# Optimization experiments

Measured on AMD Instinct MI355X. Metric: run time of the kernel, lower is better.

The kernel has to match this reference:

```python
import jax, jax.numpy as jnp
import numpy as np

NUM_HEADS = 16
NUM_KV_HEADS = 4
HEAD_DIM = 128
BATCH = 4
SEQ = 2048  # equal per-sequence length; cu_seqlens = arange(BATCH+1)*SEQ


def setup_inputs() -> dict:
    key = jax.random.key(0)
    k1, k2, k3 = jax.random.split(key, 3)
    T = BATCH * SEQ
    q = jax.random.normal(k1, (T, NUM_HEADS * HEAD_DIM), dtype=jnp.float32)
    k = jax.random.normal(k2, (T, NUM_KV_HEADS * HEAD_DIM), dtype=jnp.float32)
    v = jax.random.normal(k3, (T, NUM_KV_HEADS * HEAD_DIM), dtype=jnp.float32)
    cu = jnp.arange(BATCH + 1, dtype=jnp.int32) * SEQ
    return {"q": q, "k": k, "v": v, "cu_seqlens_q": cu, "cu_seqlens_k": cu}


def reference(q, k, v, cu_seqlens_q, cu_seqlens_k):
    # Prefill varlen causal attention with GQA (block_tables=None path).
    # Sequences have equal length, so the ragged batch reshapes to dense [B,S,...].
    B = cu_seqlens_q.shape[0] - 1
    T = q.shape[0]
    S = T // B
    D = HEAD_DIM
    G = NUM_HEADS // NUM_KV_HEADS  # GQA group size
    qh = q.reshape(B, S, NUM_KV_HEADS, G, D)
    kh = k.reshape(B, S, NUM_KV_HEADS, D)
    vh = v.reshape(B, S, NUM_KV_HEADS, D)
    scale = 1.0 / np.sqrt(D).astype(np.float32)  # SDPA scale=None default
    # scores: [B, Hkv, G, Sq, Sk]
    scores = jnp.einsum('bqhgd,bkhd->bhgqk', qh, kh) * scale
    causal = jnp.tril(jnp.ones((S, S), dtype=bool))
    scores = jnp.where(causal, scores, jnp.finfo(scores.dtype).min)
    probs = jax.nn.softmax(scores, axis=-1)
    o = jnp.einsum('bhgqk,bkhd->bqhgd', probs, vh)
    return o.reshape(T, NUM_HEADS * HEAD_DIM)
```

## Files before the change

### kernel.cpp

```cpp
#include <hip/hip_runtime.h>


typedef __attribute__((ext_vector_type(8))) short bs8;
typedef __attribute__((ext_vector_type(16))) float f16x;
typedef __attribute__((ext_vector_type(4))) unsigned int u32x4;
typedef __attribute__((ext_vector_type(4))) unsigned short u16x4;
typedef unsigned short u16;
typedef unsigned int u32;

#define B_ 4
#define S_ 2048
#define HQ_ 16
#define HKV_ 4
#define NQT 16
#define NKT_TOT 32
#define TILE_ELEMS 8192

__device__ __forceinline__ u16 f2bf(float f) {
  u32 u = __float_as_uint(f);
  u += 0x7fffu + ((u >> 16) & 1u);
  return (u16)(u >> 16);
}

__global__ void pack_k(const float* __restrict__ k, u16* __restrict__ kp) {
  int g = blockIdx.x * 256 + threadIdx.x;
  int row = g >> 7;
  int col = (g & 127) << 2;
  int h = col >> 7, d0 = col & 127;
  int b = row >> 11, s = row & 2047;
  int kt = s >> 6, kv = s & 63;
  float4 vv = *(const float4*)(k + (size_t)row * 512 + col);
  int ti = (b * HKV_ + h) * NKT_TOT + kt;
  int e = kv * 128 + (d0 ^ (8 * (kv & 15)));
  u16x4 o;
  o.x = f2bf(vv.x); o.y = f2bf(vv.y); o.z = f2bf(vv.z); o.w = f2bf(vv.w);
  *(u16x4*)(kp + (size_t)ti * TILE_ELEMS + e) = o;
}

__global__ void pack_v(const float* __restrict__ v, u16* __restrict__ vp) {
  __shared__ u16 img[TILE_ELEMS];
  int ti = blockIdx.x;
  int kt = ti & 31;
  int bh = ti >> 5;
  int h = bh & 3, b = bh >> 2;
  int t = threadIdx.x;
#pragma unroll
  for (int p = 0; p < 8; ++p) {
    int t2 = p * 256 + t;
    int kvr = t2 >> 5;
    int d0 = (t2 & 31) << 2;
    float4 vv = *(const float4*)(v + (size_t)(b * S_ + kt * 64 + kvr) * 512 + h * 128 + d0);
    float a[4] = {vv.x, vv.y, vv.z, vv.w};
#pragma unroll
    for (int j = 0; j < 4; ++j) {
      int d = d0 + j;
      img[(d >> 1) * 128 + (d & 1) * 64 + (kvr ^ (8 * ((d >> 1) & 7)))] = f2bf(a[j]);
    }
  }
  __syncthreads();
#pragma unroll
  for (int p = 0; p < 4; ++p) {
    int e0 = (p * 256 + t) * 8;
    *(bs8*)(vp + (size_t)ti * TILE_ELEMS + e0) = *(const bs8*)&img[e0];
  }
}

__device__ __forceinline__ void gl2lds(const u16* g, u16* l) {
  __builtin_amdgcn_global_load_lds((const __attribute__((address_space(1))) void*)g,
                                   (__attribute__((address_space(3))) void*)l,
                                   16, 0, 0);
}

__global__ __launch_bounds__(512, 2) void attn_fwd(
    const float* __restrict__ q, const u16* __restrict__ kp,
    const u16* __restrict__ vp, float* __restrict__ out) {
  __shared__ u16 Ks[2][TILE_ELEMS];
  __shared__ u16 Vs[2][TILE_ELEMS];

  const int bx = blockIdx.x;
  const int qt = (bx < 256) ? (15 - (bx >> 5)) : ((bx >> 5) - 8);
  const int rest = bx & 31;
  const int b = rest >> 3, hkv = (rest >> 1) & 3, gp = rest & 1;
  const int w = threadIdx.x >> 6, lane = threadIdx.x & 63;
  const int wq = w & 3;
  const int hq = hkv * 4 + gp * 2 + (w >> 2);
  const int l31 = lane & 31, hi = lane >> 5;
  const int q0 = qt * 128;
  const float scale2 = 0.08838834764831845f * 1.4426950408889634f;

  bs8 qf[8];
  {
    int row = b * S_ + q0 + wq * 32 + l31;
    const float* qrow = q + (size_t)row * 2048 + hq * 128;
#pragma unroll
    for (int ki = 0; ki < 8; ++ki) {
      const float* p0 = qrow + ki * 16 + hi * 8;
      float4 a = *(const float4*)p0;
      float4 c = *(const float4*)(p0 + 4);
      bs8 f;
      f[0] = (short)f2bf(a.x * scale2); f[1] = (short)f2bf(a.y * scale2);
      f[2] = (short)f2bf(a.z * scale2); f[3] = (short)f2bf(a.w * scale2);
      f[4] = (short)f2bf(c.x * scale2); f[5] = (short)f2bf(c.y * scale2);
      f[6] = (short)f2bf(c.z * scale2); f[7] = (short)f2bf(c.w * scale2);
      qf[ki] = f;
    }
  }

  f16x O[4];
#pragma unroll
  for (int dt = 0; dt < 4; ++dt)
#pragma unroll
    for (int e = 0; e < 16; ++e) O[dt][e] = 0.f;
  float m_run = -1e30f, l_run = 0.f;

  const size_t tbase = (size_t)((b * HKV_ + hkv) * NKT_TOT) * TILE_ELEMS;
  const u16* kbase = kp + tbase;
  const u16* vbase = vp + tbase;
  const int nkt = 2 * qt + 2;
  const int myrowmax = q0 + wq * 32 + 31;
  const int qpos = q0 + wq * 32 + l31;

  const int swzk = 8 * (l31 & 15);
  const int swzv = 8 * ((l31 >> 1) & 7);
  const int vrowbase = (l31 >> 1) * 128 + (l31 & 1) * 64;

  const int cbase = (w & 3) * 4;
  const bool stageK = (w < 4);

#pragma unroll
  for (int j = 0; j < 4; ++j) {
    int c = cbase + j;
    if (stageK) gl2lds(kbase + c * 512 + lane * 8, &Ks[0][c * 512]);
    else        gl2lds(vbase + c * 512 + lane * 8, &Vs[0][c * 512]);
  }
  asm volatile("s_waitcnt vmcnt(0)" ::: "memory");
  __syncthreads();

  int cur = 0;
  for (int t = 0; t < nkt; ++t) {
    if (t + 1 < nkt) {
      const u16* kg = kbase + (size_t)(t + 1) * TILE_ELEMS;
      const u16* vg = vbase + (size_t)(t + 1) * TILE_ELEMS;
#pragma unroll
      for (int j = 0; j < 4; ++j) {
        int c = cbase + j;
        if (stageK) gl2lds(kg + c * 512 + lane * 8, &Ks[cur ^ 1][c * 512]);
        else        gl2lds(vg + c * 512 + lane * 8, &Vs[cur ^ 1][c * 512]);
      }
    }

    if (t * 64 <= myrowmax) {
      f16x Sa[2];
#pragma unroll
      for (int kb = 0; kb < 2; ++kb)
#pragma unroll
        for (int e = 0; e < 16; ++e) Sa[kb][e] = 0.f;

      __builtin_amdgcn_s_setprio(1);
#pragma unroll
      for (int ki = 0; ki < 8; ++ki) {
        int koff = (ki * 16 + hi * 8) ^ swzk;
#pragma unroll
        for (int kb = 0; kb < 2; ++kb) {
          bs8 kf = *(const bs8*)&Ks[cur][(kb * 32 + l31) * 128 + koff];
          Sa[kb] = __builtin_amdgcn_mfma_f32_32x32x16_bf16(kf, qf[ki], Sa[kb], 0, 0, 0);
        }
      }
      __builtin_amdgcn_s_setprio(0);

      if (t >= 2 * qt) {
#pragma unroll
        for (int kb = 0; kb < 2; ++kb)
#pragma unroll
          for (int r = 0; r < 16; ++r) {
            int kvpos = t * 64 + kb * 32 + (r & 3) + 8 * (r >> 2) + 4 * hi;
            if (kvpos > qpos) Sa[kb][r] = -1e30f;
          }
      }

      float tm[8];
#pragma unroll
      for (int r = 0; r < 8; ++r)
        tm[r] = fmaxf(fmaxf(Sa[0][r], Sa[0][r + 8]), fmaxf(Sa[1][r], Sa[1][r + 8]));
#pragma unroll
      for (int s = 4; s > 0; s >>= 1)
#pragma unroll
        for (int r = 0; r < s; ++r) tm[r] = fmaxf(tm[r], tm[r + s]);
      float pmax = fmaxf(tm[0], __shfl_xor(tm[0], 32, 64));

      if (__any(pmax > m_run + 8.0f)) {
        float mnew = fmaxf(m_run, pmax);
        float alpha = exp2f(m_run - mnew);
        m_run = mnew;
        l_run *= alpha;
#pragma unroll
        for (int r = 0; r < 16; ++r) {
          float ar = __shfl(alpha, (r & 3) + 8 * (r >> 2) + 4 * hi, 64);
#pragma unroll
          for (int dt = 0; dt < 4; ++dt) O[dt][r] *= ar;
        }
      }

#pragma unroll
      for (int kb = 0; kb < 2; ++kb)
#pragma unroll
        for (int r = 0; r < 16; ++r) Sa[kb][r] = exp2f(Sa[kb][r] - m_run);
      float ts[8];
#pragma unroll
      for (int r = 0; r < 8; ++r)
        ts[r] = (Sa[0][r] + Sa[0][r + 8]) + (Sa[1][r] + Sa[1][r + 8]);
#pragma unroll
      for (int s = 4; s > 0; s >>= 1)
#pragma unroll
        for (int r = 0; r < s; ++r) ts[r] += ts[r + s];
      l_run += ts[0];

      bs8 pf[2][2];
#pragma unroll
      for (int kb = 0; kb < 2; ++kb) {
        u32 pk_[8];
#pragma unroll
        for (int j = 0; j < 8; ++j) {
          float lo = Sa[kb][2 * j], hif = Sa[kb][2 * j + 1];
          asm("v_cvt_pk_bf16_f32 %0, %1, %2" : "=v"(pk_[j]) : "v"(lo), "v"(hif));
        }
#pragma unroll
        for (int ks = 0; ks < 2; ++ks) {
          auto s0 = __builtin_amdgcn_permlane32_swap((int)pk_[4 * ks], (int)pk_[4 * ks + 2], false, false);
          auto s1 = __builtin_amdgcn_permlane32_swap((int)pk_[4 * ks + 1], (int)pk_[4 * ks + 3], false, false);
          u32x4 fw;
          fw[0] = (u32)s0[0]; fw[1] = (u32)s1[0]; fw[2] = (u32)s0[1]; fw[3] = (u32)s1[1];
          pf[kb][ks] = __builtin_bit_cast(bs8, fw);
        }
      }

      __builtin_amdgcn_s_setprio(1);
#pragma unroll
      for (int dt = 0; dt < 4; ++dt) {
#pragma unroll
        for (int kb = 0; kb < 2; ++kb)
#pragma unroll
          for (int ks = 0; ks < 2; ++ks) {
            int kvoff = (kb * 32 + ks * 16 + hi * 8) ^ swzv;
            bs8 vb = *(const bs8*)&Vs[cur][dt * 2048 + vrowbase + kvoff];
            O[dt] = __builtin_amdgcn_mfma_f32_32x32x16_bf16(pf[kb][ks], vb, O[dt], 0, 0, 0);
          }
      }
      __builtin_amdgcn_s_setprio(0);
    }

    asm volatile("s_waitcnt vmcnt(0)" ::: "memory");
    __syncthreads();
    cur ^= 1;
  }

  float lt = l_run + __shfl_xor(l_run, 32, 64);
  float inv = 1.0f / lt;
  const int orow0 = b * S_ + q0 + wq * 32;
#pragma unroll
  for (int r = 0; r < 16; ++r) {
    int qr = (r & 3) + 8 * (r >> 2) + 4 * hi;
    float li = __shfl(inv, qr, 64);
    float* op = out + (size_t)(orow0 + qr) * 2048 + hq * 128 + l31;
#pragma unroll
    for (int dt = 0; dt < 4; ++dt) op[dt * 32] = O[dt][r] * li;
  }
}

extern "C" void kernel_launch(void* const* d_in, const int* in_sizes, int n_in,
                              void* d_out, int out_size, void* d_ws, size_t ws_size,
                              hipStream_t stream) {
  const float* q = (const float*)d_in[0];
  const float* k = (const float*)d_in[1];
  const float* v = (const float*)d_in[2];
  float* out = (float*)d_out;
  u16* kp = (u16*)d_ws;
  u16* vp = kp + (size_t)B_ * HKV_ * NKT_TOT * TILE_ELEMS;

  pack_k<<<(B_ * S_ * 512 / 4) / 256, 256, 0, stream>>>(k, kp);
  pack_v<<<B_ * HKV_ * NKT_TOT, 256, 0, stream>>>(v, vp);
  attn_fwd<<<512, 512, 0, stream>>>(q, kp, vp, out);
}
```

Baseline: 133.8 us.

## Use one head per block with single-buffered K/V tiles and more resident blocks

Before, each 512-thread block handled two query heads that shared one KV head, and K/V tiles were double-buffered in LDS. Now each 256-thread block handles a single query head, K/V tiles are single-buffered with a load-wait-sync before compute, and launch bounds allow four blocks per CU. This halves LDS per block and drops the load-balancing block order in favour of a simple longest-first qt order. The cost is that K/V tiles are no longer shared across two heads, so global/L2 traffic for K/V doubles, and load latency is now exposed inside each block and can only be hidden by other resident blocks.

```diff
diff --git a/kernel.cpp b/kernel.cpp
--- a/kernel.cpp
+++ b/kernel.cpp
@@ -71,26 +71,24 @@
                                    16, 0, 0);
 }
 
-__global__ __launch_bounds__(512, 2) void attn_fwd(
+__global__ __launch_bounds__(256, 4) void attn_fwd(
     const float* __restrict__ q, const u16* __restrict__ kp,
     const u16* __restrict__ vp, float* __restrict__ out) {
-  __shared__ u16 Ks[2][TILE_ELEMS];
-  __shared__ u16 Vs[2][TILE_ELEMS];
+  __shared__ u16 Ks[TILE_ELEMS];
+  __shared__ u16 Vs[TILE_ELEMS];
 
   const int bx = blockIdx.x;
-  const int qt = (bx < 256) ? (15 - (bx >> 5)) : ((bx >> 5) - 8);
-  const int rest = bx & 31;
-  const int b = rest >> 3, hkv = (rest >> 1) & 3, gp = rest & 1;
+  const int qt = (NQT - 1) - (bx >> 6);
+  const int bh = bx & 63;
+  const int b = bh >> 4, hq = bh & 15, hkv = hq >> 2;
   const int w = threadIdx.x >> 6, lane = threadIdx.x & 63;
-  const int wq = w & 3;
-  const int hq = hkv * 4 + gp * 2 + (w >> 2);
   const int l31 = lane & 31, hi = lane >> 5;
   const int q0 = qt * 128;
   const float scale2 = 0.08838834764831845f * 1.4426950408889634f;
 
   bs8 qf[8];
   {
-    int row = b * S_ + q0 + wq * 32 + l31;
+    int row = b * S_ + q0 + w * 32 + l31;
     const float* qrow = q + (size_t)row * 2048 + hq * 128;
 #pragma unroll
     for (int ki = 0; ki < 8; ++ki) {
@@ -117,37 +115,27 @@
   const u16* kbase = kp + tbase;
   const u16* vbase = vp + tbase;
   const int nkt = 2 * qt + 2;
-  const int myrowmax = q0 + wq * 32 + 31;
-  const int qpos = q0 + wq * 32 + l31;
+  const int myrowmax = q0 + w * 32 + 31;
+  const int qpos = q0 + w * 32 + l31;
 
   const int swzk = 8 * (l31 & 15);
   const int swzv = 8 * ((l31 >> 1) & 7);
   const int vrowbase = (l31 >> 1) * 128 + (l31 & 1) * 64;
 
-  const int cbase = (w & 3) * 4;
-  const bool stageK = (w < 4);
-
-#pragma unroll
-  for (int j = 0; j < 4; ++j) {
-    int c = cbase + j;
-    if (stageK) gl2lds(kbase + c * 512 + lane * 8, &Ks[0][c * 512]);
-    else        gl2lds(vbase + c * 512 + lane * 8, &Vs[0][c * 512]);
-  }
-  asm volatile("s_waitcnt vmcnt(0)" ::: "memory");
-  __syncthreads();
-
-  int cur = 0;
   for (int t = 0; t < nkt; ++t) {
-    if (t + 1 < nkt) {
-      const u16* kg = kbase + (size_t)(t + 1) * TILE_ELEMS;
-      const u16* vg = vbase + (size_t)(t + 1) * TILE_ELEMS;
+    __syncthreads();
+    {
+      const u16* kg = kbase + (size_t)t * TILE_ELEMS;
+      const u16* vg = vbase + (size_t)t * TILE_ELEMS;
 #pragma unroll
       for (int j = 0; j < 4; ++j) {
-        int c = cbase + j;
-        if (stageK) gl2lds(kg + c * 512 + lane * 8, &Ks[cur ^ 1][c * 512]);
-        else        gl2lds(vg + c * 512 + lane * 8, &Vs[cur ^ 1][c * 512]);
-      }
-    }
+        int c = w * 4 + j;
+        gl2lds(kg + c * 512 + lane * 8, &Ks[c * 512]);
+        gl2lds(vg + c * 512 + lane * 8, &Vs[c * 512]);
+      }
+    }
+    asm volatile("s_waitcnt vmcnt(0)" ::: "memory");
+    __syncthreads();
 
     if (t * 64 <= myrowmax) {
       f16x Sa[2];
@@ -162,7 +150,7 @@
         int koff = (ki * 16 + hi * 8) ^ swzk;
 #pragma unroll
         for (int kb = 0; kb < 2; ++kb) {
-          bs8 kf = *(const bs8*)&Ks[cur][(kb * 32 + l31) * 128 + koff];
+          bs8 kf = *(const bs8*)&Ks[(kb * 32 + l31) * 128 + koff];
           Sa[kb] = __builtin_amdgcn_mfma_f32_32x32x16_bf16(kf, qf[ki], Sa[kb], 0, 0, 0);
         }
       }
@@ -242,21 +230,17 @@
 #pragma unroll
           for (int ks = 0; ks < 2; ++ks) {
             int kvoff = (kb * 32 + ks * 16 + hi * 8) ^ swzv;
-            bs8 vb = *(const bs8*)&Vs[cur][dt * 2048 + vrowbase + kvoff];
+            bs8 vb = *(const bs8*)&Vs[dt * 2048 + vrowbase + kvoff];
             O[dt] = __builtin_amdgcn_mfma_f32_32x32x16_bf16(pf[kb][ks], vb, O[dt], 0, 0, 0);
           }
       }
       __builtin_amdgcn_s_setprio(0);
     }
-
-    asm volatile("s_waitcnt vmcnt(0)" ::: "memory");
-    __syncthreads();
-    cur ^= 1;
   }
 
   float lt = l_run + __shfl_xor(l_run, 32, 64);
   float inv = 1.0f / lt;
-  const int orow0 = b * S_ + q0 + wq * 32;
+  const int orow0 = b * S_ + q0 + w * 32;
 #pragma unroll
   for (int r = 0; r < 16; ++r) {
     int qr = (r & 3) + 8 * (r >> 2) + 4 * hi;
@@ -279,5 +263,5 @@
 
   pack_k<<<(B_ * S_ * 512 / 4) / 256, 256, 0, stream>>>(k, kp);
   pack_v<<<B_ * HKV_ * NKT_TOT, 256, 0, stream>>>(v, vp);
-  attn_fwd<<<512, 512, 0, stream>>>(q, kp, vp, out);
-}
+  attn_fwd<<<B_ * HQ_ * NQT, 256, 0, stream>>>(q, kp, vp, out);
+}
```

Result: slower. 185.5 us (+38.6%).
